# Kernel optimization log

Measured on AMD Instinct MI355X. Metric: run time of the kernel, lower is better.

Reference implementation:

```python
import jax, jax.numpy as jnp
import numpy as np

B_SZ = 8
D_MODEL = 512
D_STATE = 64
N2 = D_STATE // 2  # S4D uses complex-conjugate pairs -> d_state//2 complex modes
L_SEQ = 2048


def setup_inputs() -> dict:
    key = jax.random.key(0)
    ks = jax.random.split(key, 16)
    d = D_MODEL
    scale = 1.0 / np.sqrt(d)
    inp = {
        "x": jax.random.normal(ks[0], (B_SZ, d, L_SEQ), dtype=jnp.float32),
        # q/k/v projections (nn.Linear: weight (out,in), bias (out,))
        "Wq": jax.random.normal(ks[1], (d, d), dtype=jnp.float32) * scale,
        "bq": jax.random.normal(ks[2], (d,), dtype=jnp.float32) * scale,
        "Wk": jax.random.normal(ks[3], (d, d), dtype=jnp.float32) * scale,
        "bk": jax.random.normal(ks[4], (d,), dtype=jnp.float32) * scale,
        "Wv": jax.random.normal(ks[5], (d, d), dtype=jnp.float32) * scale,
        "bv": jax.random.normal(ks[6], (d,), dtype=jnp.float32) * scale,
        # Shift layer params
        "shift_C": jax.random.normal(ks[7], (1, d, D_STATE), dtype=jnp.float32),
        "shift_D": jax.random.normal(ks[8], (d,), dtype=jnp.float32),
        # S4D (diagonal SSM) params
        "log_dt": jax.random.uniform(ks[9], (d,), dtype=jnp.float32,
                                      minval=np.log(1e-3), maxval=np.log(1e-1)),
        "A_real": jnp.log(0.5 * jnp.ones((d, N2), dtype=jnp.float32)),
        "A_imag": jnp.broadcast_to(np.pi * jnp.arange(N2, dtype=jnp.float32), (d, N2)),
        "C_re": jax.random.normal(ks[10], (d, N2), dtype=jnp.float32) * np.sqrt(0.5),
        "C_im": jax.random.normal(ks[11], (d, N2), dtype=jnp.float32) * np.sqrt(0.5),
        "s4_D": jax.random.normal(ks[12], (d,), dtype=jnp.float32),
    }
    return inp


def _linear_chan(x, W, b):
    # x: (B, H, L); Linear applied over channel dim H -> (B, H_out, L)
    return jnp.einsum("bhl,dh->bdl", x, W) + b[:, None]


def _shift(u, C, Dp):
    """Shift SSM: causal conv with kernel = first L taps of C (computed via FFT
    exactly as the torch source does). u: (B, H, L)."""
    L = u.shape[-1]
    n = 2 * L
    H, S = C.shape[1], C.shape[2]
    Bmat = jnp.zeros((H, S), dtype=u.dtype).at[:, 0].set(1.0)
    B_fc = jnp.conj(jnp.fft.rfft(Bmat, n=n, axis=-1))  # (H, L+1)
    C_f = jnp.fft.rfft(C, n=n, axis=-1)                # (1, H, L+1)
    kernel = jnp.fft.irfft(B_fc * C_f, n=n, axis=-1)[..., :L]  # (1, H, L)
    kernel_f = jnp.fft.rfft(kernel, n=n, axis=-1)      # (1, H, L+1)
    u_f = jnp.fft.rfft(u, n=n, axis=-1)                # (B, H, L+1)
    y = jnp.fft.irfft(u_f * kernel_f, n=n, axis=-1)[..., :L]
    return y + u * Dp[:, None]


def _s4d(u, log_dt, A_real, A_imag, C_re, C_im, Dp):
    """Standard S4D forward: ZOH-discretized diagonal SSM kernel + FFT conv.
    u: (B, H, L)."""
    L = u.shape[-1]
    n = 2 * L
    dt = jnp.exp(log_dt)[:, None]                  # (H, 1)
    A = -jnp.exp(A_real) + 1j * A_imag             # (H, N2)
    dtA = A * dt                                   # (H, N2)
    C = (C_re + 1j * C_im) * (jnp.exp(dtA) - 1.0) / A
    vand = jnp.exp(dtA[:, :, None] * jnp.arange(L))  # (H, N2, L)
    K = 2.0 * jnp.einsum("hn,hnl->hl", C, vand).real  # (H, L)
    y = jnp.fft.irfft(jnp.fft.rfft(u, n=n, axis=-1) * jnp.fft.rfft(K, n=n, axis=-1),
                      n=n, axis=-1)[..., :L]
    return y + u * Dp[:, None]


def reference(x, Wq, bq, Wk, bk, Wv, bv, shift_C, shift_D,
              log_dt, A_real, A_imag, C_re, C_im, s4_D):
    q = _linear_chan(x, Wq, bq)
    k = _linear_chan(x, Wk, bk)
    v = _linear_chan(x, Wv, bv)
    shift_out = _shift(k, shift_C, shift_D)
    s4d_out = _s4d(v * shift_out, log_dt, A_real, A_imag, C_re, C_im, s4_D)
    return q * s4d_out
```

## Files before the change

### kernel.cpp

```cpp
#include <hip/hip_runtime.h>
#include <cstdint>


#define DMODEL 512
#define LSEQ 2048

typedef _Float16 half_t;
typedef __attribute__((ext_vector_type(2))) _Float16 half2v;
typedef __attribute__((ext_vector_type(4))) _Float16 half4v;
typedef __attribute__((ext_vector_type(8))) _Float16 half8v;
typedef __attribute__((ext_vector_type(4))) float floatx4;

#define SW(R, c) ((R) * 64 + ((((c) >> 3) ^ ((R) & 7)) << 3) + ((c) & 7))

__device__ __forceinline__ void gload_lds16(const half_t* g, half_t* l) {
  __builtin_amdgcn_global_load_lds(
      (const __attribute__((address_space(1))) uint32_t*)g,
      (__attribute__((address_space(3))) uint32_t*)l, 16, 0, 0);
}

#define WAIT_LGKM_BAR()                                   \
  do {                                                    \
    asm volatile("s_waitcnt lgkmcnt(0)" ::: "memory");    \
    __builtin_amdgcn_s_barrier();                         \
    __builtin_amdgcn_sched_barrier(0);                    \
  } while (0)

__global__ __launch_bounds__(256) void prep(
    const float* __restrict__ x, const float* __restrict__ Wq,
    const float* __restrict__ Wk, const float* __restrict__ Wv,
    const float* __restrict__ log_dt, const float* __restrict__ A_real,
    const float* __restrict__ A_imag, const float* __restrict__ C_re,
    const float* __restrict__ C_im, const float* __restrict__ shC,
    half_t* __restrict__ xT, half_t* __restrict__ W16,
    half_t* __restrict__ Vt, half_t* __restrict__ Et, half_t* __restrict__ Tt,
    half_t* __restrict__ T1t, half_t* __restrict__ T2t,
    float* __restrict__ wt2) {
  __shared__ float tile[64][68];
  __shared__ float aL[32], bL[32], wrL[32], wiL[32], crL[32], ciL[32];
  __shared__ float Kt[64], tapl[64];
  int bid = blockIdx.x;
  int tid = threadIdx.x;

  if (bid < 512) {
    int h = bid;
    if (tid < 64) { Kt[tid] = 0.f; tapl[tid] = shC[h * 64 + tid]; }
    if (tid < 32) {
      int n = tid, hn = h * 32 + n;
      float dt = expf(log_dt[h]);
      float Ar = -expf(A_real[hn]), Ai = A_imag[hn];
      float a = dt * Ar, b = dt * Ai;
      float ea = expf(a);
      float wr = ea * cosf(b), wi = ea * sinf(b);
      float Am2 = Ar * Ar + Ai * Ai;
      float zr = wr - 1.0f, zi = wi;
      float qr = (zr * Ar + zi * Ai) / Am2;
      float qi = (zi * Ar - zr * Ai) / Am2;
      aL[n] = a; bL[n] = b; wrL[n] = wr; wiL[n] = wi;
      crL[n] = C_re[hn] * qr - C_im[hn] * qi;
      ciL[n] = C_re[hn] * qi + C_im[hn] * qr;
      float e64 = expf(64.0f * a);
      wt2[h * 64 + 2 * n]     = e64 * cosf(64.0f * b);
      wt2[h * 64 + 2 * n + 1] = e64 * sinf(64.0f * b);
    }
    __syncthreads();
    size_t base = (size_t)h * 4096;
    {
      int r = tid >> 2;
      int nb = (tid & 3) * 8;
      float ksum = 0.f;
#pragma unroll
      for (int i = 0; i < 8; i++) {
        int n = nb + i;
        float a = aL[n], b = bL[n];
        float cr = crL[n], ci = ciL[n];
        float er = expf(a * (float)r);
        float w0r = er * cosf(b * (float)r), w0i = er * sinf(b * (float)r);
        ksum += 2.f * (cr * w0r - ci * w0i);
        float wr = wrL[n], wi = wiL[n];
        float w1r = w0r * wr - w0i * wi, w1i = w0r * wi + w0i * wr;
        Et[base + SW(r, 2 * n)]     = (half_t)(2.f * (cr * w1r - ci * w1i));
        Et[base + SW(r, 2 * n + 1)] = (half_t)(-2.f * (cr * w1i + ci * w1r));
        Vt[base + SW(2 * n, 63 - r)]     = (half_t)w0r;
        Vt[base + SW(2 * n + 1, 63 - r)] = (half_t)w0i;
      }
      atomicAdd(&Kt[r], ksum);
    }
    __syncthreads();
#pragma unroll
    for (int e = 0; e < 16; e++) {
      int idx = e * 256 + tid;
      int r = idx >> 6, t = idx & 63;
      int d = r - t;
      size_t a = base + SW(r, t);
      Tt[a]  = (d >= 0) ? (half_t)Kt[d] : (half_t)0.f;
      T1t[a] = (d >= 0) ? (half_t)tapl[d] : (half_t)0.f;
      T2t[a] = (d < 0) ? (half_t)tapl[64 + d] : (half_t)0.f;
    }
  } else if (bid < 2560) {
    int i = bid - 512;
    int b = i >> 8, rem = i & 255;
    int d0 = (rem >> 5) * 64, l0 = (rem & 31) * 64;
    int dy = tid >> 4, lx = tid & 15;
    const float* xp = x + ((size_t)(b * 512 + d0)) * 2048 + l0;
#pragma unroll
    for (int rr = 0; rr < 4; rr++) {
      float4 v = *(const float4*)(xp + (size_t)(rr * 16 + dy) * 2048 + lx * 4);
      *(float4*)&tile[rr * 16 + dy][lx * 4] = v;
    }
    __syncthreads();
    half_t* op = xT + ((size_t)(b * 2048 + l0)) * 512 + d0;
    int lr = tid >> 2, c4 = tid & 3;
#pragma unroll
    for (int cc = 0; cc < 2; cc++) {
      int ch = cc * 4 + c4;
      half8v hv;
#pragma unroll
      for (int e = 0; e < 8; e++) hv[e] = (half_t)tile[ch * 8 + e][lr];
      *(half8v*)(op + (size_t)lr * 512 + ch * 8) = hv;
    }
  } else {
    int base = (bid - 2560) * 256 + tid;
#pragma unroll
    for (int it = 0; it < 6; it++) {
      int i = base + it * 131072;
      const float* src = (i < 262144) ? Wq : ((i < 524288) ? Wk : Wv);
      W16[i] = (half_t)src[i & 262143];
    }
  }
}

__global__ __launch_bounds__(256) void gemm_qkv(
    const half_t* __restrict__ xT, const half_t* __restrict__ Wstk,
    const float* __restrict__ bq, const float* __restrict__ bk,
    const float* __restrict__ bv, half_t* __restrict__ outq,
    half_t* __restrict__ outk, half_t* __restrict__ outv) {
  __shared__ half_t smem[16384];
  half_t* As = smem;
  half_t* Bs = smem + 8192;
  int flat = blockIdx.x;
  int swz = (flat & 7) * 192 + (flat >> 3);
  int nt = swz / 12, mt = swz - nt * 12;
  int n0 = nt * 128, m0 = mt * 128;
  int tid = threadIdx.x;
  int lane = tid & 63, wid = tid >> 6;
  int wr = wid >> 1, wc = wid & 1;
  int lrow = lane & 15, lg = lane >> 4;
  int rsub = lane >> 3, ssub = lane & 7;
  int gslot = ssub ^ rsub;

  floatx4 acc[4][4];
#pragma unroll
  for (int i = 0; i < 4; i++)
#pragma unroll
    for (int j = 0; j < 4; j++) acc[i][j] = (floatx4){0.f, 0.f, 0.f, 0.f};

  const half_t* gA = Wstk + (size_t)(m0 + wid * 32 + rsub) * 512 + gslot * 8;
  const half_t* gB = xT + (size_t)(n0 + wid * 32 + rsub) * 512 + gslot * 8;

  for (int kk = 0; kk < 512; kk += 64) {
#pragma unroll
    for (int i = 0; i < 4; i++) {
      int c = wid * 4 + i;
      gload_lds16(gA + (size_t)i * 8 * 512 + kk, As + c * 512);
      gload_lds16(gB + (size_t)i * 8 * 512 + kk, Bs + c * 512);
    }
    __syncthreads();
#pragma unroll
    for (int h = 0; h < 2; h++) {
      half8v af[4], bf[4];
#pragma unroll
      for (int i = 0; i < 4; i++) {
        int r = wr * 64 + i * 16 + lrow;
        af[i] = *(const half8v*)(As + r * 64 + ((h * 4 + lg) ^ (r & 7)) * 8);
      }
#pragma unroll
      for (int j = 0; j < 4; j++) {
        int r = wc * 64 + j * 16 + lrow;
        bf[j] = *(const half8v*)(Bs + r * 64 + ((h * 4 + lg) ^ (r & 7)) * 8);
      }
#pragma unroll
      for (int i = 0; i < 4; i++)
#pragma unroll
        for (int j = 0; j < 4; j++)
          acc[i][j] = __builtin_amdgcn_mfma_f32_16x16x32_f16(af[i], bf[j],
                                                             acc[i][j], 0, 0, 0);
    }
    __syncthreads();
  }

  int z = m0 >> 9;
  const float* bias = (z == 0) ? bq : ((z == 1) ? bk : bv);
  half_t* smemC = smem;
#pragma unroll
  for (int i = 0; i < 4; i++) {
    int dl = wr * 64 + i * 16 + 4 * lg;
    float4 b4 = *(const float4*)&bias[(m0 + dl) & 511];
#pragma unroll
    for (int j = 0; j < 4; j++) {
      int ll = wc * 64 + j * 16 + lrow;
#pragma unroll
      for (int reg = 0; reg < 4; reg++) {
        int d = dl + reg;
        float val = acc[i][j][reg] + ((const float*)&b4)[reg];
        smemC[d * 128 + (((ll >> 3) ^ (d & 15)) << 3) + (ll & 7)] = (half_t)val;
      }
    }
  }
  __syncthreads();
  {
    int t4 = tid >> 4, ch = tid & 15;
    int b = n0 >> 11, l0 = n0 & 2047;
    half_t* outp = (z == 0) ? outq : ((z == 1) ? outk : outv);
#pragma unroll
    for (int rep = 0; rep < 8; rep++) {
      int d = rep * 16 + t4;
      half8v v = *(const half8v*)(smemC + d * 128 + ((ch ^ (d & 15)) << 3));
      size_t rowb = ((size_t)(b * 512 + ((m0 + d) & 511))) * 2048;
      if (z == 0) {
        *(half8v*)(outp + rowb + l0 + ch * 8) = v;
      } else {
        int j = (l0 >> 6) + (ch >> 3);
        int s = ch & 7;
        *(half8v*)(outp + rowb + j * 64 + ((s ^ (j & 7)) << 3)) = v;
      }
    }
  }
}

__global__ __launch_bounds__(256) void s4d_main(
    const half_t* __restrict__ kimg, const half_t* __restrict__ vimg,
    const half_t* __restrict__ T1t, const half_t* __restrict__ T2t,
    const half_t* __restrict__ Vt, const half_t* __restrict__ Et,
    const half_t* __restrict__ Tt, const float* __restrict__ wt2,
    const float* __restrict__ shD, const float* __restrict__ s4D,
    const half_t* __restrict__ qbuf, float* __restrict__ outp) {
  __shared__ half_t kl[33 * 64];
  __shared__ half_t vg[32 * 64];
  __shared__ half_t uh[32 * 64];
  __shared__ half_t tabA[4096];
  __shared__ half_t tabB[4096];
  __shared__ half_t tabC[4096];
  __shared__ float SG[32 * 66];
  int swz = (blockIdx.x & 7) * 512 + (blockIdx.x >> 3);
  int h = swz >> 3, bi = swz & 7;
  int bh = bi * 512 + h;
  int tid = threadIdx.x;
  int lane = tid & 63, wid = tid >> 6;
  int lrow = lane & 15, lg = lane >> 4;
  int mi = wid & 1, ri0 = wid >> 1;

  {
    size_t tb = (size_t)h * 4096;
    gload_lds16(kimg + (size_t)bh * 2048 + wid * 512 + lane * 8,
                kl + 64 + wid * 512);
    gload_lds16(vimg + (size_t)bh * 2048 + wid * 512 + lane * 8,
                vg + wid * 512);
#pragma unroll
    for (int i = 0; i < 2; i++) {
      int c = wid * 2 + i;
      gload_lds16(T1t + tb + c * 512 + lane * 8, tabA + c * 512);
      gload_lds16(T2t + tb + c * 512 + lane * 8, tabB + c * 512);
      gload_lds16(Vt + tb + c * 512 + lane * 8, tabC + c * 512);
    }
  }
  if (tid < 8) {
    half8v zz = {(_Float16)0, (_Float16)0, (_Float16)0, (_Float16)0,
                 (_Float16)0, (_Float16)0, (_Float16)0, (_Float16)0};
    *(half8v*)(kl + tid * 8) = zz;
  }
  float sDsh = shD[h];
  float sD4 = s4D[h];
  float wTr = wt2[h * 64 + 2 * (tid & 31)];
  float wTi = wt2[h * 64 + 2 * (tid & 31) + 1];
  asm volatile("s_waitcnt vmcnt(0) lgkmcnt(0)" ::: "memory");
  __builtin_amdgcn_s_barrier();
  __builtin_amdgcn_sched_barrier(0);

#define LDF(base, r, ks, key) \
  (*(const half8v*)((base) + (r) * 64 + (((ks) * 4 + lg) ^ (key)) * 8))

  floatx4 acc[2];
  acc[0] = (floatx4){0.f, 0.f, 0.f, 0.f};
  acc[1] = (floatx4){0.f, 0.f, 0.f, 0.f};
  {
    int jA = mi * 16 + lrow;
    int key1 = lrow & 7, key2 = (lrow + 7) & 7;
#pragma unroll
    for (int ks = 0; ks < 2; ks++) {
      half8v a1 = LDF(kl, 1 + jA, ks, key1);
      half8v a2 = LDF(kl, jA, ks, key2);
#pragma unroll
      for (int tt = 0; tt < 2; tt++) {
        int rb = (ri0 + tt * 2) * 16 + lrow;
        half8v b1 = LDF(tabA, rb, ks, lrow & 7);
        half8v b2 = LDF(tabB, rb, ks, lrow & 7);
        acc[tt] = __builtin_amdgcn_mfma_f32_16x16x32_f16(a1, b1, acc[tt], 0, 0, 0);
        acc[tt] = __builtin_amdgcn_mfma_f32_16x16x32_f16(a2, b2, acc[tt], 0, 0, 0);
      }
    }
  }
#pragma unroll
  for (int tt = 0; tt < 2; tt++) {
#pragma unroll
    for (int reg = 0; reg < 4; reg++) {
      int j = mi * 16 + 4 * lg + reg;
      int r = (ri0 + tt * 2) * 16 + lrow;
      int cph = (((r >> 3) ^ (j & 7)) << 3) + (r & 7);
      float kvv = (float)kl[(1 + j) * 64 + cph];
      float vvv = (float)vg[j * 64 + cph];
      uh[j * 64 + cph] = (half_t)(vvv * (acc[tt][reg] + sDsh * kvv));
    }
  }
  WAIT_LGKM_BAR();

  {
    size_t tb = (size_t)h * 4096;
#pragma unroll
    for (int i = 0; i < 2; i++) {
      int c = wid * 2 + i;
      gload_lds16(Et + tb + c * 512 + lane * 8, tabA + c * 512);
      gload_lds16(Tt + tb + c * 512 + lane * 8, tabB + c * 512);
    }
  }

  acc[0] = (floatx4){0.f, 0.f, 0.f, 0.f};
  acc[1] = (floatx4){0.f, 0.f, 0.f, 0.f};
#pragma unroll
  for (int ks = 0; ks < 2; ks++) {
    half8v a = LDF(uh, mi * 16 + lrow, ks, lrow & 7);
#pragma unroll
    for (int tt = 0; tt < 2; tt++) {
      int rb = (ri0 + tt * 2) * 16 + lrow;
      half8v b = LDF(tabC, rb, ks, lrow & 7);
      acc[tt] = __builtin_amdgcn_mfma_f32_16x16x32_f16(a, b, acc[tt], 0, 0, 0);
    }
  }
#pragma unroll
  for (int tt = 0; tt < 2; tt++) {
    int ri = ri0 + tt * 2;
#pragma unroll
    for (int reg = 0; reg < 4; reg++) {
      int j = mi * 16 + 4 * lg + reg;
      SG[j * 66 + ri * 16 + lrow] = acc[tt][reg];
    }
  }
  asm volatile("s_waitcnt vmcnt(0) lgkmcnt(0)" ::: "memory");
  __builtin_amdgcn_s_barrier();
  __builtin_amdgcn_sched_barrier(0);

  if (tid < 32) {
    int n = tid;
    float gr = 0.f, gi = 0.f;
#pragma unroll 4
    for (int j = 0; j < 32; j++) {
      float tr = SG[j * 66 + 2 * n], ti = SG[j * 66 + 2 * n + 1];
      half2v gp = {(half_t)gr, (half_t)gi};
      *(half2v*)(vg + j * 64 + (((n >> 2) ^ (j & 7)) << 3) + 2 * (n & 3)) = gp;
      float nr = wTr * gr - wTi * gi + tr;
      gi = wTr * gi + wTi * gr + ti;
      gr = nr;
    }
  }
  WAIT_LGKM_BAR();

  acc[0] = (floatx4){0.f, 0.f, 0.f, 0.f};
  acc[1] = (floatx4){0.f, 0.f, 0.f, 0.f};
#pragma unroll
  for (int ks = 0; ks < 2; ks++) {
    half8v ag = LDF(vg, mi * 16 + lrow, ks, lrow & 7);
    half8v au = LDF(uh, mi * 16 + lrow, ks, lrow & 7);
#pragma unroll
    for (int tt = 0; tt < 2; tt++) {
      int rb = (ri0 + tt * 2) * 16 + lrow;
      half8v be = LDF(tabA, rb, ks, lrow & 7);
      half8v bt = LDF(tabB, rb, ks, lrow & 7);
      acc[tt] = __builtin_amdgcn_mfma_f32_16x16x32_f16(ag, be, acc[tt], 0, 0, 0);
      acc[tt] = __builtin_amdgcn_mfma_f32_16x16x32_f16(au, bt, acc[tt], 0, 0, 0);
    }
  }
#pragma unroll
  for (int tt = 0; tt < 2; tt++) {
#pragma unroll
    for (int reg = 0; reg < 4; reg++) {
      int j = mi * 16 + 4 * lg + reg;
      int r = (ri0 + tt * 2) * 16 + lrow;
      int cph = (((r >> 3) ^ (j & 7)) << 3) + (r & 7);
      SG[j * 64 + r] = acc[tt][reg] + sD4 * (float)uh[j * 64 + cph];
    }
  }
  WAIT_LGKM_BAR();

  {
    size_t base = (size_t)bh * 2048;
    half8v qv = *(const half8v*)(qbuf + base + tid * 8);
    float* op = outp + base;
    float4 o0, o1;
    o0.x = (float)qv[0] * SG[tid * 8 + 0];
    o0.y = (float)qv[1] * SG[tid * 8 + 1];
    o0.z = (float)qv[2] * SG[tid * 8 + 2];
    o0.w = (float)qv[3] * SG[tid * 8 + 3];
    o1.x = (float)qv[4] * SG[tid * 8 + 4];
    o1.y = (float)qv[5] * SG[tid * 8 + 5];
    o1.z = (float)qv[6] * SG[tid * 8 + 6];
    o1.w = (float)qv[7] * SG[tid * 8 + 7];
    *(float4*)(op + tid * 8) = o0;
    *(float4*)(op + tid * 8 + 4) = o1;
  }
#undef LDF
}

extern "C" void kernel_launch(void* const* d_in, const int* in_sizes, int n_in,
                              void* d_out, int out_size, void* d_ws, size_t ws_size,
                              hipStream_t stream) {
  const float* x      = (const float*)d_in[0];
  const float* Wq     = (const float*)d_in[1];
  const float* bq     = (const float*)d_in[2];
  const float* Wk     = (const float*)d_in[3];
  const float* bk     = (const float*)d_in[4];
  const float* Wv     = (const float*)d_in[5];
  const float* bv     = (const float*)d_in[6];
  const float* shC    = (const float*)d_in[7];
  const float* shD    = (const float*)d_in[8];
  const float* log_dt = (const float*)d_in[9];
  const float* A_real = (const float*)d_in[10];
  const float* A_imag = (const float*)d_in[11];
  const float* C_re   = (const float*)d_in[12];
  const float* C_im   = (const float*)d_in[13];
  const float* s4D    = (const float*)d_in[14];
  float* out = (float*)d_out;
  half_t* wsh = (half_t*)d_ws;

  half_t* qbuf = wsh;
  half_t* kbuf = wsh + 8388608;
  half_t* vbuf = wsh + 16777216;
  half_t* xT16 = wsh + 25165824;
  half_t* W16  = wsh + 33554432;
  half_t* Vt   = wsh + 34340864;
  half_t* Et   = wsh + 36438016;
  half_t* Tt   = wsh + 38535168;
  half_t* T1t  = wsh + 40632320;
  half_t* T2t  = wsh + 42729472;
  float*  wt2  = (float*)(wsh + 44826624);

  prep<<<3072, 256, 0, stream>>>(x, Wq, Wk, Wv, log_dt, A_real, A_imag,
                                 C_re, C_im, shC, xT16, W16,
                                 Vt, Et, Tt, T1t, T2t, wt2);
  gemm_qkv<<<dim3(1536), 256, 0, stream>>>(xT16, W16, bq, bk, bv,
                                           qbuf, kbuf, vbuf);
  s4d_main<<<4096, 256, 0, stream>>>(kbuf, vbuf, T1t, T2t, Vt, Et, Tt,
                                     wt2, shD, s4D, qbuf, out);
}
```

Baseline: 85.38 us.

## Process two batches per s4d_main block to share per-channel tables in LDS

Each s4d_main block now runs 512 threads covering two batch elements of the same channel, so the T1/T2/V and E/T tables are loaded into shared memory once and used by both halves. This halves the table traffic from global memory and halves the grid size. In exchange the block needs about 66 KB of dynamic shared memory and larger blocks, which may lower how many blocks fit per CU, and the serial scan phase still uses only 32 threads per group.

```diff
diff --git a/kernel.cpp b/kernel.cpp
--- a/kernel.cpp
+++ b/kernel.cpp
@@ -228,51 +228,55 @@
   }
 }
 
-__global__ __launch_bounds__(256) void s4d_main(
+__global__ __launch_bounds__(512) void s4d_main(
     const half_t* __restrict__ kimg, const half_t* __restrict__ vimg,
     const half_t* __restrict__ T1t, const half_t* __restrict__ T2t,
     const half_t* __restrict__ Vt, const half_t* __restrict__ Et,
     const half_t* __restrict__ Tt, const float* __restrict__ wt2,
     const float* __restrict__ shD, const float* __restrict__ s4D,
     const half_t* __restrict__ qbuf, float* __restrict__ outp) {
-  __shared__ half_t kl[33 * 64];
-  __shared__ half_t vg[32 * 64];
-  __shared__ half_t uh[32 * 64];
-  __shared__ half_t tabA[4096];
-  __shared__ half_t tabB[4096];
-  __shared__ half_t tabC[4096];
-  __shared__ float SG[32 * 66];
-  int swz = (blockIdx.x & 7) * 512 + (blockIdx.x >> 3);
-  int h = swz >> 3, bi = swz & 7;
-  int bh = bi * 512 + h;
+  extern __shared__ char smem_raw[];
+  half_t* tabA = (half_t*)smem_raw;
+  half_t* tabB = tabA + 4096;
+  half_t* tabC = tabB + 4096;
+  half_t* klb  = tabC + 4096;
+  half_t* vgb  = klb + 2 * 2112;
+  half_t* uhb  = vgb + 2 * 2048;
+  float*  SGb  = (float*)(uhb + 2 * 2048);
+  int swz = (blockIdx.x & 7) * 256 + (blockIdx.x >> 3);
+  int h = swz >> 2, bp = swz & 3;
   int tid = threadIdx.x;
   int lane = tid & 63, wid = tid >> 6;
+  int g = wid >> 2, w4 = wid & 3;
+  int tid4 = tid & 255;
+  int bi = bp * 2 + g;
+  int bh = bi * 512 + h;
   int lrow = lane & 15, lg = lane >> 4;
-  int mi = wid & 1, ri0 = wid >> 1;
+  int mi = w4 & 1, ri0 = w4 >> 1;
+  half_t* klg = klb + g * 2112;
+  half_t* vgg = vgb + g * 2048;
+  half_t* uhg = uhb + g * 2048;
+  float*  SGg = SGb + g * 2112;
 
   {
     size_t tb = (size_t)h * 4096;
-    gload_lds16(kimg + (size_t)bh * 2048 + wid * 512 + lane * 8,
-                kl + 64 + wid * 512);
-    gload_lds16(vimg + (size_t)bh * 2048 + wid * 512 + lane * 8,
-                vg + wid * 512);
-#pragma unroll
-    for (int i = 0; i < 2; i++) {
-      int c = wid * 2 + i;
-      gload_lds16(T1t + tb + c * 512 + lane * 8, tabA + c * 512);
-      gload_lds16(T2t + tb + c * 512 + lane * 8, tabB + c * 512);
-      gload_lds16(Vt + tb + c * 512 + lane * 8, tabC + c * 512);
-    }
-  }
-  if (tid < 8) {
+    gload_lds16(kimg + (size_t)bh * 2048 + w4 * 512 + lane * 8,
+                klg + 64 + w4 * 512);
+    gload_lds16(vimg + (size_t)bh * 2048 + w4 * 512 + lane * 8,
+                vgg + w4 * 512);
+    gload_lds16(T1t + tb + wid * 512 + lane * 8, tabA + wid * 512);
+    gload_lds16(T2t + tb + wid * 512 + lane * 8, tabB + wid * 512);
+    gload_lds16(Vt  + tb + wid * 512 + lane * 8, tabC + wid * 512);
+  }
+  if (tid4 < 8) {
     half8v zz = {(_Float16)0, (_Float16)0, (_Float16)0, (_Float16)0,
                  (_Float16)0, (_Float16)0, (_Float16)0, (_Float16)0};
-    *(half8v*)(kl + tid * 8) = zz;
+    *(half8v*)(klg + tid4 * 8) = zz;
   }
   float sDsh = shD[h];
   float sD4 = s4D[h];
-  float wTr = wt2[h * 64 + 2 * (tid & 31)];
-  float wTi = wt2[h * 64 + 2 * (tid & 31) + 1];
+  float wTr = wt2[h * 64 + 2 * (tid4 & 31)];
+  float wTi = wt2[h * 64 + 2 * (tid4 & 31) + 1];
   asm volatile("s_waitcnt vmcnt(0) lgkmcnt(0)" ::: "memory");
   __builtin_amdgcn_s_barrier();
   __builtin_amdgcn_sched_barrier(0);
@@ -288,8 +292,8 @@
     int key1 = lrow & 7, key2 = (lrow + 7) & 7;
 #pragma unroll
     for (int ks = 0; ks < 2; ks++) {
-      half8v a1 = LDF(kl, 1 + jA, ks, key1);
-      half8v a2 = LDF(kl, jA, ks, key2);
+      half8v a1 = LDF(klg, 1 + jA, ks, key1);
+      half8v a2 = LDF(klg, jA, ks, key2);
 #pragma unroll
       for (int tt = 0; tt < 2; tt++) {
         int rb = (ri0 + tt * 2) * 16 + lrow;
@@ -307,28 +311,24 @@
       int j = mi * 16 + 4 * lg + reg;
       int r = (ri0 + tt * 2) * 16 + lrow;
       int cph = (((r >> 3) ^ (j & 7)) << 3) + (r & 7);
-      float kvv = (float)kl[(1 + j) * 64 + cph];
-      float vvv = (float)vg[j * 64 + cph];
-      uh[j * 64 + cph] = (half_t)(vvv * (acc[tt][reg] + sDsh * kvv));
+      float kvv = (float)klg[(1 + j) * 64 + cph];
+      float vvv = (float)vgg[j * 64 + cph];
+      uhg[j * 64 + cph] = (half_t)(vvv * (acc[tt][reg] + sDsh * kvv));
     }
   }
   WAIT_LGKM_BAR();
 
   {
     size_t tb = (size_t)h * 4096;
-#pragma unroll
-    for (int i = 0; i < 2; i++) {
-      int c = wid * 2 + i;
-      gload_lds16(Et + tb + c * 512 + lane * 8, tabA + c * 512);
-      gload_lds16(Tt + tb + c * 512 + lane * 8, tabB + c * 512);
-    }
+    gload_lds16(Et + tb + wid * 512 + lane * 8, tabA + wid * 512);
+    gload_lds16(Tt + tb + wid * 512 + lane * 8, tabB + wid * 512);
   }
 
   acc[0] = (floatx4){0.f, 0.f, 0.f, 0.f};
   acc[1] = (floatx4){0.f, 0.f, 0.f, 0.f};
 #pragma unroll
   for (int ks = 0; ks < 2; ks++) {
-    half8v a = LDF(uh, mi * 16 + lrow, ks, lrow & 7);
+    half8v a = LDF(uhg, mi * 16 + lrow, ks, lrow & 7);
 #pragma unroll
     for (int tt = 0; tt < 2; tt++) {
       int rb = (ri0 + tt * 2) * 16 + lrow;
@@ -342,21 +342,21 @@
 #pragma unroll
     for (int reg = 0; reg < 4; reg++) {
       int j = mi * 16 + 4 * lg + reg;
-      SG[j * 66 + ri * 16 + lrow] = acc[tt][reg];
+      SGg[j * 66 + ri * 16 + lrow] = acc[tt][reg];
     }
   }
   asm volatile("s_waitcnt vmcnt(0) lgkmcnt(0)" ::: "memory");
   __builtin_amdgcn_s_barrier();
   __builtin_amdgcn_sched_barrier(0);
 
-  if (tid < 32) {
-    int n = tid;
+  if (tid4 < 32) {
+    int n = tid4;
     float gr = 0.f, gi = 0.f;
 #pragma unroll 4
     for (int j = 0; j < 32; j++) {
-      float tr = SG[j * 66 + 2 * n], ti = SG[j * 66 + 2 * n + 1];
+      float tr = SGg[j * 66 + 2 * n], ti = SGg[j * 66 + 2 * n + 1];
       half2v gp = {(half_t)gr, (half_t)gi};
-      *(half2v*)(vg + j * 64 + (((n >> 2) ^ (j & 7)) << 3) + 2 * (n & 3)) = gp;
+      *(half2v*)(vgg + j * 64 + (((n >> 2) ^ (j & 7)) << 3) + 2 * (n & 3)) = gp;
       float nr = wTr * gr - wTi * gi + tr;
       gi = wTr * gi + wTi * gr + ti;
       gr = nr;
@@ -368,8 +368,8 @@
   acc[1] = (floatx4){0.f, 0.f, 0.f, 0.f};
 #pragma unroll
   for (int ks = 0; ks < 2; ks++) {
-    half8v ag = LDF(vg, mi * 16 + lrow, ks, lrow & 7);
-    half8v au = LDF(uh, mi * 16 + lrow, ks, lrow & 7);
+    half8v ag = LDF(vgg, mi * 16 + lrow, ks, lrow & 7);
+    half8v au = LDF(uhg, mi * 16 + lrow, ks, lrow & 7);
 #pragma unroll
     for (int tt = 0; tt < 2; tt++) {
       int rb = (ri0 + tt * 2) * 16 + lrow;
@@ -386,26 +386,26 @@
       int j = mi * 16 + 4 * lg + reg;
       int r = (ri0 + tt * 2) * 16 + lrow;
       int cph = (((r >> 3) ^ (j & 7)) << 3) + (r & 7);
-      SG[j * 64 + r] = acc[tt][reg] + sD4 * (float)uh[j * 64 + cph];
+      SGg[j * 64 + r] = acc[tt][reg] + sD4 * (float)uhg[j * 64 + cph];
     }
   }
   WAIT_LGKM_BAR();
 
   {
     size_t base = (size_t)bh * 2048;
-    half8v qv = *(const half8v*)(qbuf + base + tid * 8);
+    half8v qv = *(const half8v*)(qbuf + base + tid4 * 8);
     float* op = outp + base;
     float4 o0, o1;
-    o0.x = (float)qv[0] * SG[tid * 8 + 0];
-    o0.y = (float)qv[1] * SG[tid * 8 + 1];
-    o0.z = (float)qv[2] * SG[tid * 8 + 2];
-    o0.w = (float)qv[3] * SG[tid * 8 + 3];
-    o1.x = (float)qv[4] * SG[tid * 8 + 4];
-    o1.y = (float)qv[5] * SG[tid * 8 + 5];
-    o1.z = (float)qv[6] * SG[tid * 8 + 6];
-    o1.w = (float)qv[7] * SG[tid * 8 + 7];
-    *(float4*)(op + tid * 8) = o0;
-    *(float4*)(op + tid * 8 + 4) = o1;
+    o0.x = (float)qv[0] * SGg[tid4 * 8 + 0];
+    o0.y = (float)qv[1] * SGg[tid4 * 8 + 1];
+    o0.z = (float)qv[2] * SGg[tid4 * 8 + 2];
+    o0.w = (float)qv[3] * SGg[tid4 * 8 + 3];
+    o1.x = (float)qv[4] * SGg[tid4 * 8 + 4];
+    o1.y = (float)qv[5] * SGg[tid4 * 8 + 5];
+    o1.z = (float)qv[6] * SGg[tid4 * 8 + 6];
+    o1.w = (float)qv[7] * SGg[tid4 * 8 + 7];
+    *(float4*)(op + tid4 * 8) = o0;
+    *(float4*)(op + tid4 * 8 + 4) = o1;
   }
 #undef LDF
 }
@@ -443,11 +443,14 @@
   half_t* T2t  = wsh + 42729472;
   float*  wt2  = (float*)(wsh + 44826624);
 
+  hipFuncSetAttribute((const void*)s4d_main,
+                      hipFuncAttributeMaxDynamicSharedMemorySize, 66304);
+
   prep<<<3072, 256, 0, stream>>>(x, Wq, Wk, Wv, log_dt, A_real, A_imag,
                                  C_re, C_im, shC, xT16, W16,
                                  Vt, Et, Tt, T1t, T2t, wt2);
   gemm_qkv<<<dim3(1536), 256, 0, stream>>>(xT16, W16, bq, bk, bv,
                                            qbuf, kbuf, vbuf);
-  s4d_main<<<4096, 256, 0, stream>>>(kbuf, vbuf, T1t, T2t, Vt, Et, Tt,
-                                     wt2, shD, s4D, qbuf, out);
+  s4d_main<<<dim3(2048), 512, 66304, stream>>>(kbuf, vbuf, T1t, T2t, Vt, Et,
+                                               Tt, wt2, shD, s4D, qbuf, out);
 }
```

After: 85.39 us. Within noise of the previous version (+0.0%).
